# Optimization experiments

Hardware: AMD Instinct MI355X
Metric: run time of the kernel (lower is better)

## Reference

```python
import jax, jax.numpy as jnp
import numpy as np


def _gru_layer(x_seq, W_ih, W_hh, b_ih, b_hh):
    # x_seq: [B, T, D_in]; PyTorch gate order: r, z, n
    B, T, _ = x_seq.shape
    H = W_hh.shape[1]
    # Precompute input-to-hidden gates for all timesteps (one big GEMM)
    gx = jnp.einsum('btd,gd->btg', x_seq, W_ih) + b_ih  # [B, T, 3H]

    def step(h, gx_t):
        gh = h @ W_hh.T + b_hh  # [B, 3H]
        r = jax.nn.sigmoid(gx_t[:, :H] + gh[:, :H])
        z = jax.nn.sigmoid(gx_t[:, H:2 * H] + gh[:, H:2 * H])
        n = jnp.tanh(gx_t[:, 2 * H:] + r * gh[:, 2 * H:])
        h_new = (1.0 - z) * n + z * h
        return h_new, h_new

    h0 = jnp.zeros((B, H), dtype=x_seq.dtype)
    _, hs = jax.lax.scan(step, h0, jnp.swapaxes(gx, 0, 1))  # hs: [T, B, H]
    return jnp.swapaxes(hs, 0, 1)  # [B, T, H]


def setup_inputs() -> dict:
    key = jax.random.key(0)
    ks = jax.random.split(key, 11)
    B, T, D, H, O = 64, 512, 128, 512, 1
    s_ih0 = 1.0 / np.sqrt(D)
    s_h = 1.0 / np.sqrt(H)
    return {
        'X': jax.random.normal(ks[0], (B, T, D), dtype=jnp.float32),
        'W_ih0': jax.random.normal(ks[1], (3 * H, D), dtype=jnp.float32) * s_ih0,
        'W_hh0': jax.random.normal(ks[2], (3 * H, H), dtype=jnp.float32) * s_h,
        'b_ih0': jax.random.normal(ks[3], (3 * H,), dtype=jnp.float32) * s_h,
        'b_hh0': jax.random.normal(ks[4], (3 * H,), dtype=jnp.float32) * s_h,
        'W_ih1': jax.random.normal(ks[5], (3 * H, H), dtype=jnp.float32) * s_h,
        'W_hh1': jax.random.normal(ks[6], (3 * H, H), dtype=jnp.float32) * s_h,
        'b_ih1': jax.random.normal(ks[7], (3 * H,), dtype=jnp.float32) * s_h,
        'b_hh1': jax.random.normal(ks[8], (3 * H,), dtype=jnp.float32) * s_h,
        'W_fc': jax.random.normal(ks[9], (O, H), dtype=jnp.float32) * s_h,
        'b_fc': jax.random.normal(ks[10], (O,), dtype=jnp.float32) * s_h,
    }


def reference(X, W_ih0, W_hh0, b_ih0, b_hh0, W_ih1, W_hh1, b_ih1, b_hh1, W_fc, b_fc):
    h1 = _gru_layer(X, W_ih0, W_hh0, b_ih0, b_hh0)     # [B, T, H]
    h2 = _gru_layer(h1, W_ih1, W_hh1, b_ih1, b_hh1)    # [B, T, H]
    out = h2[:, -1, :] @ W_fc.T + b_fc                 # [B, O]
    return out
```

## Files before the change

### kernel.cpp

```cpp
#include <hip/hip_runtime.h>
#include <math.h>

#define B_  64
#define T_  512
#define D0_ 128
#define H_  512
#define G3_ 1536
#define HSTR 512
#define BSTR 528
#define BKg 32
#define SENT 0x7FC00000u

typedef short short8 __attribute__((ext_vector_type(8)));
typedef float f32x4 __attribute__((ext_vector_type(4)));
typedef unsigned uint32x4 __attribute__((ext_vector_type(4)));

__device__ __forceinline__ float fast_sig(float x) {
  return __builtin_amdgcn_rcpf(1.f + __expf(-x));
}
__device__ __forceinline__ float fast_tanh(float x) {
  return 1.f - 2.f * __builtin_amdgcn_rcpf(1.f + __expf(2.f * x));
}

__device__ __forceinline__ unsigned short f2bf_rne(float f) {
  unsigned u = __float_as_uint(f);
  unsigned r = (u + 0x7fffu + ((u >> 16) & 1u)) >> 16;
  return (unsigned short)r;
}
__device__ __forceinline__ float bf2f(unsigned short h) {
  return __uint_as_float(((unsigned)h) << 16);
}

__global__ __launch_bounds__(768, 3) void scan_kernel(
    const unsigned short* __restrict__ WhH, const unsigned short* __restrict__ WhL,
    const float* __restrict__ bhh,
    const float* __restrict__ gx, float* __restrict__ hist,
    int t0, int tc, int gxt0, int gxT)
{
  __shared__ float hsh[4 * HSTR];
  __shared__ unsigned short hbh[4 * BSTR];
  __shared__ unsigned short hbl[4 * BSTR];
  __shared__ float ghp[4][96 * 5];
  __shared__ float bsh[96];

  const int tid = threadIdx.x;
  const int blk = blockIdx.x;
  const int g = blk >> 4, c = blk & 15;
  const int j0 = c << 5;
  const int bbase = g << 2;

  const int wv = tid >> 6, lane = tid & 63;
  const int q = wv & 3, p = wv >> 2;
  const int rloc = lane & 15, kq = lane >> 4;
  const int rowA = 32 * p + rloc;
  const int rowB = 32 * p + 16 + rloc;
  const int wrowA = (rowA >> 5) * H_ + j0 + (rowA & 31);
  const int wrowB = (rowB >> 5) * H_ + j0 + (rowB & 31);

  short8 whA[4], wlA[4], whB[4], wlB[4];
  {
    const unsigned short* RHA = WhH + (size_t)wrowA * H_ + q * 128 + (kq << 3);
    const unsigned short* RLA = WhL + (size_t)wrowA * H_ + q * 128 + (kq << 3);
    const unsigned short* RHB = WhH + (size_t)wrowB * H_ + q * 128 + (kq << 3);
    const unsigned short* RLB = WhL + (size_t)wrowB * H_ + q * 128 + (kq << 3);
    #pragma unroll
    for (int cc = 0; cc < 4; ++cc) {
      whA[cc] = *(const short8*)(RHA + cc * 32);
      wlA[cc] = *(const short8*)(RLA + cc * 32);
      whB[cc] = *(const short8*)(RHB + cc * 32);
      wlB[cc] = *(const short8*)(RLB + cc * 32);
    }
  }
  if (tid < 96)
    bsh[tid] = bhh[(tid >> 5) * H_ + j0 + (tid & 31)];

  size_t go0 = 0;
  if (tid < 128) {
    int bb = tid >> 5, j = tid & 31;
    go0 = ((size_t)(bbase + bb) * gxT) * (size_t)G3_ + j0 + j;
  }
  __syncthreads();

  for (int t = t0; t < t0 + tc; ++t) {
    if (t == 0) {
      for (int idx = tid; idx < 2048; idx += 768) hsh[idx] = 0.f;
      for (int idx = tid; idx < 4 * BSTR; idx += 768) {
        hbh[idx] = 0; hbl[idx] = 0;
      }
    } else if (tid < 512) {
      const int bb = tid >> 7, e4 = tid & 127;
      const unsigned* qp = (const unsigned*)
          (hist + ((size_t)(bbase + bb) * T_ + (t - 1)) * H_) + (e4 << 2);
      uint32x4 v;
      for (;;) {
        asm volatile(
            "global_load_dwordx4 %0, %1, off sc0 sc1\n\t"
            "s_waitcnt vmcnt(0)"
            : "=&v"(v) : "v"(qp) : "memory");
        if (v.x != SENT && v.y != SENT && v.z != SENT && v.w != SENT) break;
      }
      float4 f = make_float4(__uint_as_float(v.x), __uint_as_float(v.y),
                             __uint_as_float(v.z), __uint_as_float(v.w));
      *(float4*)&hsh[bb * HSTR + (e4 << 2)] = f;
      unsigned short h0 = f2bf_rne(f.x), h1 = f2bf_rne(f.y),
                     h2 = f2bf_rne(f.z), h3 = f2bf_rne(f.w);
      *(ushort4*)&hbh[bb * BSTR + (e4 << 2)] = make_ushort4(h0, h1, h2, h3);
      unsigned short l0 = f2bf_rne(f.x - bf2f(h0)), l1 = f2bf_rne(f.y - bf2f(h1)),
                     l2 = f2bf_rne(f.z - bf2f(h2)), l3 = f2bf_rne(f.w - bf2f(h3));
      *(ushort4*)&hbl[bb * BSTR + (e4 << 2)] = make_ushort4(l0, l1, l2, l3);
    }

    float gxr = 0.f, gxz = 0.f, gxn = 0.f;
    if (tid < 128) {
      size_t go = go0 + (size_t)(t - gxt0) * (size_t)G3_;
      gxr = gx[go]; gxz = gx[go + 512]; gxn = gx[go + 1024];
    }
    __syncthreads();

    {
      f32x4 aHHA = (f32x4){0.f,0.f,0.f,0.f}, aHLA = aHHA, aLHA = aHHA;
      f32x4 aHHB = aHHA, aHLB = aHHA, aLHB = aHHA;
      const int bb4 = lane & 3;
      const unsigned short* bhp = hbh + bb4 * BSTR + q * 128 + (kq << 3);
      const unsigned short* blp = hbl + bb4 * BSTR + q * 128 + (kq << 3);
      #pragma unroll
      for (int cc = 0; cc < 4; ++cc) {
        short8 bh = *(const short8*)(bhp + cc * 32);
        short8 bl = *(const short8*)(blp + cc * 32);
        aHHA = __builtin_amdgcn_mfma_f32_16x16x32_bf16(whA[cc], bh, aHHA, 0, 0, 0);
        aHHB = __builtin_amdgcn_mfma_f32_16x16x32_bf16(whB[cc], bh, aHHB, 0, 0, 0);
        aHLA = __builtin_amdgcn_mfma_f32_16x16x32_bf16(whA[cc], bl, aHLA, 0, 0, 0);
        aHLB = __builtin_amdgcn_mfma_f32_16x16x32_bf16(whB[cc], bl, aHLB, 0, 0, 0);
        aLHA = __builtin_amdgcn_mfma_f32_16x16x32_bf16(wlA[cc], bh, aLHA, 0, 0, 0);
        aLHB = __builtin_amdgcn_mfma_f32_16x16x32_bf16(wlB[cc], bh, aLHB, 0, 0, 0);
      }
      f32x4 accA = (aHHA + aHLA) + aLHA;
      f32x4 accB = (aHHB + aHLB) + aLHB;
      if (rloc < 4) {
        #pragma unroll
        for (int r = 0; r < 4; ++r)
          ghp[q][((2 * p) * 16 + (kq << 2) + r) * 5 + rloc] = accA[r];
        #pragma unroll
        for (int r = 0; r < 4; ++r)
          ghp[q][((2 * p + 1) * 16 + (kq << 2) + r) * 5 + rloc] = accB[r];
      }
    }
    __syncthreads();

    if (tid < 128) {
      int bb = tid >> 5, j = tid & 31;
      float ghr = (ghp[0][ j       * 5 + bb] + ghp[1][ j       * 5 + bb]) +
                  (ghp[2][ j       * 5 + bb] + ghp[3][ j       * 5 + bb]) + bsh[j];
      float ghz = (ghp[0][(32 + j) * 5 + bb] + ghp[1][(32 + j) * 5 + bb]) +
                  (ghp[2][(32 + j) * 5 + bb] + ghp[3][(32 + j) * 5 + bb]) + bsh[32 + j];
      float ghn = (ghp[0][(64 + j) * 5 + bb] + ghp[1][(64 + j) * 5 + bb]) +
                  (ghp[2][(64 + j) * 5 + bb] + ghp[3][(64 + j) * 5 + bb]) + bsh[64 + j];
      float rg = fast_sig(gxr + ghr);
      float zg = fast_sig(gxz + ghz);
      float ng = fast_tanh(gxn + rg * ghn);
      float hp = hsh[bb * HSTR + j0 + j];
      float hnew = (1.f - zg) * ng + zg * hp;
      __hip_atomic_store(
          (unsigned*)(hist + ((size_t)(bbase + bb) * T_ + t) * H_) + j0 + j,
          __float_as_uint(hnew), __ATOMIC_RELAXED, __HIP_MEMORY_SCOPE_AGENT);
    }
    __syncthreads();
  }
}

__global__ __launch_bounds__(256) void sent_fill(float* hist, int t0, int tc) {
  int i = blockIdx.x * 256 + threadIdx.x;
  int per = tc * (H_ >> 2);
  if (i < B_ * per) {
    int b = i / per, r = i % per;
    uint4* p = (uint4*)(hist + ((size_t)b * T_ + t0) * H_) + r;
    *p = make_uint4(SENT, SENT, SENT, SENT);
  }
}

__global__ __launch_bounds__(256) void conv_split(
    const float* __restrict__ A, int lda, int t0, int tc, int ltc,
    unsigned short* __restrict__ Ah, unsigned short* __restrict__ Al)
{
  int idx = blockIdx.x * 256 + threadIdx.x;
  int m = idx / (lda >> 2), kq = idx % (lda >> 2);
  const float4 v = *(const float4*)
      (A + ((size_t)(m >> ltc) * T_ + t0 + (m & (tc - 1))) * lda + (kq << 2));
  unsigned short h0 = f2bf_rne(v.x), h1 = f2bf_rne(v.y),
                 h2 = f2bf_rne(v.z), h3 = f2bf_rne(v.w);
  unsigned short l0 = f2bf_rne(v.x - bf2f(h0)), l1 = f2bf_rne(v.y - bf2f(h1)),
                 l2 = f2bf_rne(v.z - bf2f(h2)), l3 = f2bf_rne(v.w - bf2f(h3));
  size_t o = (size_t)m * lda + (kq << 2);
  *(ushort4*)(Ah + o) = make_ushort4(h0, h1, h2, h3);
  *(ushort4*)(Al + o) = make_ushort4(l0, l1, l2, l3);
}

__global__ __launch_bounds__(256, 2) void gemm_mfma(
    const unsigned short* __restrict__ Ah, const unsigned short* __restrict__ Al,
    const unsigned short* __restrict__ Bh, const unsigned short* __restrict__ Bl,
    const float* __restrict__ bias, float* __restrict__ gxout, int K)
{
  __shared__ unsigned short sAh[2][128 * BKg], sAl[2][128 * BKg];
  __shared__ unsigned short sBh[2][128 * BKg], sBl[2][128 * BKg];

  const int tid = threadIdx.x;
  const int m0 = blockIdx.x << 7, n0 = blockIdx.y << 7;
  const int wave = tid >> 6, lane = tid & 63;
  const int wr = (wave & 1) << 6, wc = (wave >> 1) << 6;
  const int fm = lane & 15, kh = lane >> 4;

  const int srow = tid >> 2, sq = tid & 3;
  const int lofs0 = srow * BKg + (sq << 3);
  const int lofs1 = (64 + srow) * BKg + (sq << 3);

  f32x4 acc[4][4];
  #pragma unroll
  for (int i = 0; i < 4; ++i)
    #pragma unroll
    for (int j = 0; j < 4; ++j)
      acc[i][j] = (f32x4){0.f, 0.f, 0.f, 0.f};

  float4 pAh[2], pAl[2], pBh[2], pBl[2];
  #define PREFETCH(k0)                                                        \
    {                                                                         \
      size_t a0 = (size_t)(m0 + srow) * K + (k0) + (sq << 3);                 \
      size_t a1 = (size_t)(m0 + 64 + srow) * K + (k0) + (sq << 3);            \
      size_t b0 = (size_t)(n0 + srow) * K + (k0) + (sq << 3);                 \
      size_t b1 = (size_t)(n0 + 64 + srow) * K + (k0) + (sq << 3);            \
      pAh[0] = *(const float4*)&Ah[a0]; pAh[1] = *(const float4*)&Ah[a1];     \
      pAl[0] = *(const float4*)&Al[a0]; pAl[1] = *(const float4*)&Al[a1];     \
      pBh[0] = *(const float4*)&Bh[b0]; pBh[1] = *(const float4*)&Bh[b1];     \
      pBl[0] = *(const float4*)&Bl[b0]; pBl[1] = *(const float4*)&Bl[b1];     \
    }
  #define STORE_LDS(buf)                                                      \
    {                                                                         \
      *(float4*)&sAh[buf][lofs0] = pAh[0]; *(float4*)&sAh[buf][lofs1] = pAh[1];\
      *(float4*)&sAl[buf][lofs0] = pAl[0]; *(float4*)&sAl[buf][lofs1] = pAl[1];\
      *(float4*)&sBh[buf][lofs0] = pBh[0]; *(float4*)&sBh[buf][lofs1] = pBh[1];\
      *(float4*)&sBl[buf][lofs0] = pBl[0]; *(float4*)&sBl[buf][lofs1] = pBl[1];\
    }

  PREFETCH(0);
  STORE_LDS(0);
  int buf = 0;

  for (int k0 = 0; k0 < K; k0 += BKg) {
    __syncthreads();
    const bool more = (k0 + BKg) < K;
    if (more) PREFETCH(k0 + BKg);

    short8 fAh[4], fAl[4], fBh[4], fBl[4];
    #pragma unroll
    for (int i = 0; i < 4; ++i) {
      int ao = (wr + i * 16 + fm) * BKg + (kh << 3);
      int bo = (wc + i * 16 + fm) * BKg + (kh << 3);
      fAh[i] = *(const short8*)&sAh[buf][ao];
      fAl[i] = *(const short8*)&sAl[buf][ao];
      fBh[i] = *(const short8*)&sBh[buf][bo];
      fBl[i] = *(const short8*)&sBl[buf][bo];
    }
    #pragma unroll
    for (int i = 0; i < 4; ++i)
      #pragma unroll
      for (int j = 0; j < 4; ++j) {
        acc[i][j] = __builtin_amdgcn_mfma_f32_16x16x32_bf16(
            fAh[i], fBh[j], acc[i][j], 0, 0, 0);
        acc[i][j] = __builtin_amdgcn_mfma_f32_16x16x32_bf16(
            fAh[i], fBl[j], acc[i][j], 0, 0, 0);
        acc[i][j] = __builtin_amdgcn_mfma_f32_16x16x32_bf16(
            fAl[i], fBh[j], acc[i][j], 0, 0, 0);
      }
    if (more) {
      STORE_LDS(buf ^ 1);
      buf ^= 1;
    }
  }

  #pragma unroll
  for (int j = 0; j < 4; ++j) {
    int col = n0 + wc + j * 16 + fm;
    float bv = bias[col];
    #pragma unroll
    for (int i = 0; i < 4; ++i) {
      int rowb = m0 + wr + i * 16 + (kh << 2);
      #pragma unroll
      for (int r = 0; r < 4; ++r)
        gxout[(size_t)(rowb + r) * G3_ + col] = acc[i][j][r] + bv;
    }
  }
}

__global__ void fc_kernel(const float* __restrict__ hist, const float* __restrict__ Wfc,
                          const float* __restrict__ bfc, float* __restrict__ out)
{
  int b = blockIdx.x, lane = threadIdx.x;
  const float* h = hist + ((size_t)b*T_ + (T_-1))*H_;
  float acc = 0.f;
  for (int j = lane; j < H_; j += 64) acc += h[j]*Wfc[j];
  #pragma unroll
  for (int off = 32; off; off >>= 1) acc += __shfl_down(acc, off, 64);
  if (lane == 0) out[b] = acc + bfc[0];
}

extern "C" void kernel_launch(void* const* d_in, const int* in_sizes, int n_in,
                              void* d_out, int out_size, void* d_ws, size_t ws_size,
                              hipStream_t stream)
{
  const float* X    = (const float*)d_in[0];
  const float* Wih0 = (const float*)d_in[1];
  const float* Whh0 = (const float*)d_in[2];
  const float* bih0 = (const float*)d_in[3];
  const float* bhh0 = (const float*)d_in[4];
  const float* Wih1 = (const float*)d_in[5];
  const float* Whh1 = (const float*)d_in[6];
  const float* bih1 = (const float*)d_in[7];
  const float* bhh1 = (const float*)d_in[8];
  const float* Wfc  = (const float*)d_in[9];
  const float* bfc  = (const float*)d_in[10];

  float* hist = (float*)((char*)d_ws + 4096);
  const size_t histB = (size_t)B_*T_*H_*4;

  const size_t bB = (size_t)G3_ * 512 * 2;
  const size_t wB = (size_t)G3_ * H_ * 2;
  int tcg = 128;
  {
    size_t fixed = 4096 + histB + 2 * bB + 2 * wB;
    if      (ws_size >= fixed + (size_t)B_*512*((size_t)G3_*4 + 512*4)) tcg = 512;
    else if (ws_size >= fixed + (size_t)B_*256*((size_t)G3_*4 + 512*4)) tcg = 256;
  }
  int ltc = 31 - __builtin_clz((unsigned)tcg);

  float* gxbuf = (float*)((char*)d_ws + 4096 + histB);
  const size_t gxB = (size_t)B_*tcg*G3_*4;
  unsigned short* Ahb = (unsigned short*)((char*)gxbuf + gxB);
  const size_t aB = (size_t)B_*tcg*512*2;
  unsigned short* Alb = (unsigned short*)((char*)Ahb + aB);
  unsigned short* Bhb = (unsigned short*)((char*)Alb + aB);
  unsigned short* Blb = (unsigned short*)((char*)Bhb + bB);
  unsigned short* Whb = (unsigned short*)((char*)Blb + bB);
  unsigned short* Wlb = (unsigned short*)((char*)Whb + wB);

  const int sentGridFull = (B_ * T_ * (H_ >> 2) + 255) / 256;
  const int sentGridChunk = (B_ * tcg * (H_ >> 2) + 255) / 256;

  hipLaunchKernelGGL(sent_fill, dim3(sentGridFull), dim3(256), 0, stream,
                     hist, 0, T_);

  for (int lay = 0; lay < 2; ++lay) {
    const float* A   = lay ? (const float*)hist : X;
    int lda          = lay ? H_ : D0_;
    const float* Wih = lay ? Wih1 : Wih0;
    const float* bih = lay ? bih1 : bih0;
    const float* Whh = lay ? Whh1 : Whh0;
    const float* bhh = lay ? bhh1 : bhh0;

    hipLaunchKernelGGL(conv_split, dim3((G3_*lda/4)/256), dim3(256), 0, stream,
                       Wih, lda, 0, 1 << 30, 30, Bhb, Blb);
    hipLaunchKernelGGL(conv_split, dim3((G3_*H_/4)/256), dim3(256), 0, stream,
                       Whh, H_, 0, 1 << 30, 30, Whb, Wlb);

    for (int t0g = 0; t0g < T_; t0g += tcg) {
      int M = B_ * tcg;
      hipLaunchKernelGGL(conv_split, dim3((M*lda/4)/256), dim3(256), 0, stream,
                         A, lda, t0g, tcg, ltc, Ahb, Alb);
      if (lay == 1)
        hipLaunchKernelGGL(sent_fill, dim3(sentGridChunk), dim3(256), 0, stream,
                           hist, t0g, tcg);
      dim3 ggrid(M >> 7, G3_ >> 7);
      hipLaunchKernelGGL(gemm_mfma, ggrid, dim3(256), 0, stream,
                         Ahb, Alb, Bhb, Blb, bih, gxbuf, lda);
      hipLaunchKernelGGL(scan_kernel, dim3(256), dim3(768), 0, stream,
                         Whb, Wlb, bhh, (const float*)gxbuf, hist,
                         t0g, tcg, t0g, tcg);
    }
  }

  hipLaunchKernelGGL(fc_kernel, dim3(64), dim3(64), 0, stream,
                     (const float*)hist, Wfc, bfc, (float*)d_out);
}
```

Baseline: 2.596 ms.

## Keep hidden state in registers and trim per-step barrier and polling work

Each gate thread now carries its previous hidden value in a register, which removes the fp32 shared-memory copy of h. Each block writes the bf16 hi/lo split of its own output slice straight into LDS instead of polling it back from global memory. Polling moves to waves that do not compute gates. One __syncthreads per timestep is dropped by moving the barrier to just after polling. The aim is to shorten the serial critical path of each recurrent step. The gx loads now start only after that barrier, so their latency may be less hidden.

After: 2.889 ms. 1.11x slower.

```diff
diff --git a/kernel.cpp b/kernel.cpp
--- a/kernel.cpp
+++ b/kernel.cpp
@@ -37,7 +37,6 @@
     const float* __restrict__ gx, float* __restrict__ hist,
     int t0, int tc, int gxt0, int gxT)
 {
-  __shared__ float hsh[4 * HSTR];
   __shared__ unsigned short hbh[4 * BSTR];
   __shared__ unsigned short hbl[4 * BSTR];
   __shared__ float ghp[4][96 * 5];
@@ -74,23 +73,30 @@
   if (tid < 96)
     bsh[tid] = bhh[(tid >> 5) * H_ + j0 + (tid & 31)];
 
+  float hreg = 0.f;
   size_t go0 = 0;
   if (tid < 128) {
     int bb = tid >> 5, j = tid & 31;
     go0 = ((size_t)(bbase + bb) * gxT) * (size_t)G3_ + j0 + j;
-  }
+    if (t0 > 0)
+      hreg = hist[((size_t)(bbase + bb) * T_ + (t0 - 1)) * H_ + j0 + j];
+  }
+
+  const bool isPoller = (tid >= 128 && tid < 640);
+  const int pt = tid - 128;
+  const int pbb = pt >> 7, pe4 = pt & 127;
+  const bool ownQuad = (pe4 >= (j0 >> 2)) && (pe4 < (j0 >> 2) + 8);
+
   __syncthreads();
 
   for (int t = t0; t < t0 + tc; ++t) {
     if (t == 0) {
-      for (int idx = tid; idx < 2048; idx += 768) hsh[idx] = 0.f;
       for (int idx = tid; idx < 4 * BSTR; idx += 768) {
         hbh[idx] = 0; hbl[idx] = 0;
       }
-    } else if (tid < 512) {
-      const int bb = tid >> 7, e4 = tid & 127;
+    } else if (isPoller && !(ownQuad && t > t0)) {
       const unsigned* qp = (const unsigned*)
-          (hist + ((size_t)(bbase + bb) * T_ + (t - 1)) * H_) + (e4 << 2);
+          (hist + ((size_t)(bbase + pbb) * T_ + (t - 1)) * H_) + (pe4 << 2);
       uint32x4 v;
       for (;;) {
         asm volatile(
@@ -99,23 +105,22 @@
             : "=&v"(v) : "v"(qp) : "memory");
         if (v.x != SENT && v.y != SENT && v.z != SENT && v.w != SENT) break;
       }
-      float4 f = make_float4(__uint_as_float(v.x), __uint_as_float(v.y),
-                             __uint_as_float(v.z), __uint_as_float(v.w));
-      *(float4*)&hsh[bb * HSTR + (e4 << 2)] = f;
-      unsigned short h0 = f2bf_rne(f.x), h1 = f2bf_rne(f.y),
-                     h2 = f2bf_rne(f.z), h3 = f2bf_rne(f.w);
-      *(ushort4*)&hbh[bb * BSTR + (e4 << 2)] = make_ushort4(h0, h1, h2, h3);
-      unsigned short l0 = f2bf_rne(f.x - bf2f(h0)), l1 = f2bf_rne(f.y - bf2f(h1)),
-                     l2 = f2bf_rne(f.z - bf2f(h2)), l3 = f2bf_rne(f.w - bf2f(h3));
-      *(ushort4*)&hbl[bb * BSTR + (e4 << 2)] = make_ushort4(l0, l1, l2, l3);
-    }
+      float fx = __uint_as_float(v.x), fy = __uint_as_float(v.y),
+            fz = __uint_as_float(v.z), fw = __uint_as_float(v.w);
+      unsigned short h0 = f2bf_rne(fx), h1 = f2bf_rne(fy),
+                     h2 = f2bf_rne(fz), h3 = f2bf_rne(fw);
+      *(ushort4*)&hbh[pbb * BSTR + (pe4 << 2)] = make_ushort4(h0, h1, h2, h3);
+      unsigned short l0 = f2bf_rne(fx - bf2f(h0)), l1 = f2bf_rne(fy - bf2f(h1)),
+                     l2 = f2bf_rne(fz - bf2f(h2)), l3 = f2bf_rne(fw - bf2f(h3));
+      *(ushort4*)&hbl[pbb * BSTR + (pe4 << 2)] = make_ushort4(l0, l1, l2, l3);
+    }
+    __syncthreads();
 
     float gxr = 0.f, gxz = 0.f, gxn = 0.f;
     if (tid < 128) {
       size_t go = go0 + (size_t)(t - gxt0) * (size_t)G3_;
       gxr = gx[go]; gxz = gx[go + 512]; gxn = gx[go + 1024];
     }
-    __syncthreads();
 
     {
       f32x4 aHHA = (f32x4){0.f,0.f,0.f,0.f}, aHLA = aHHA, aLHA = aHHA;
@@ -158,13 +163,15 @@
       float rg = fast_sig(gxr + ghr);
       float zg = fast_sig(gxz + ghz);
       float ng = fast_tanh(gxn + rg * ghn);
-      float hp = hsh[bb * HSTR + j0 + j];
-      float hnew = (1.f - zg) * ng + zg * hp;
+      float hnew = (1.f - zg) * ng + zg * hreg;
+      hreg = hnew;
       __hip_atomic_store(
           (unsigned*)(hist + ((size_t)(bbase + bb) * T_ + t) * H_) + j0 + j,
           __float_as_uint(hnew), __ATOMIC_RELAXED, __HIP_MEMORY_SCOPE_AGENT);
-    }
-    __syncthreads();
+      unsigned short hh = f2bf_rne(hnew);
+      hbh[bb * BSTR + j0 + j] = hh;
+      hbl[bb * BSTR + j0 + j] = f2bf_rne(hnew - bf2f(hh));
+    }
   }
 }
 
```
